# Kernel tuning notes

Hardware: AMD Instinct MI355X
Metric: run time of the kernel (lower is better)

The kernel has to match this reference:

```python
import jax, jax.numpy as jnp
import numpy as np

LN_EPS = 1e-5

def _layernorm(x, g, b):
    mu = jnp.mean(x, axis=-1, keepdims=True)
    var = jnp.mean((x - mu) ** 2, axis=-1, keepdims=True)
    return (x - mu) * jax.lax.rsqrt(var + LN_EPS) * g + b

def _linear_init(k, fan_in, fan_out):
    s = 1.0 / np.sqrt(fan_in)
    kw, kb = jax.random.split(k)
    W = jax.random.uniform(kw, (fan_in, fan_out), jnp.float32, -s, s)
    b = jax.random.uniform(kb, (fan_out,), jnp.float32, -s, s)
    return W, b

def setup_inputs() -> dict:
    key = jax.random.key(0)
    ks = jax.random.split(key, 8)
    B, C, H, W = 4, 256, 64, 64
    Cout = 256
    N = H * W
    E = 16 * N
    x = jax.random.normal(ks[0], (B, C, H, W), jnp.float32)
    edge_index = jax.random.randint(ks[1], (2, E), 0, N)
    W1, b1 = _linear_init(ks[2], C, 1024)
    W2, b2 = _linear_init(ks[3], 1024, 512)
    W3, b3 = _linear_init(ks[4], 512, Cout)
    return {
        'x': x, 'edge_index': edge_index,
        'W1': W1, 'b1': b1, 'g1': jnp.ones(1024, jnp.float32), 'be1': jnp.zeros(1024, jnp.float32),
        'W2': W2, 'b2': b2, 'g2': jnp.ones(512, jnp.float32), 'be2': jnp.zeros(512, jnp.float32),
        'W3': W3, 'b3': b3, 'g_out': jnp.ones(Cout, jnp.float32), 'b_out': jnp.zeros(Cout, jnp.float32),
    }

def reference(x, edge_index, W1, b1, g1, be1, W2, b2, g2, be2, W3, b3, g_out, b_out):
    B, C, H, Wd = x.shape
    N = H * Wd
    # [B, N, C] node features (pixels as nodes)
    x_flat = x.reshape(B, C, N).transpose(0, 2, 1)
    # Dense adjacency from edge list (duplicates sum, same as sparse->to_dense).
    # Identical for every batch item, so build once and broadcast through einsum.
    A = jnp.zeros((N, N), x.dtype).at[edge_index[0], edge_index[1]].add(1.0)
    A = A + jnp.eye(N, dtype=x.dtype)  # self-loops
    deg = jnp.sum(A, axis=-1)
    d_inv_sqrt = jnp.where(deg > 0, jax.lax.rsqrt(deg), 0.0)
    A_norm = d_inv_sqrt[:, None] * A * d_inv_sqrt[None, :]
    # message passing: [N,N] @ [B,N,C] -> [B,N,C]
    h = jnp.einsum('mn,bnc->bmc', A_norm, x_flat)
    h = _layernorm(jax.nn.relu(h @ W1 + b1), g1, be1)
    h = _layernorm(jax.nn.relu(h @ W2 + b2), g2, be2)
    h = h @ W3 + b3
    h = _layernorm(h, g_out, b_out)
    return h.transpose(0, 2, 1).reshape(B, -1, H, Wd)
```

## Files before the change

kernel.cpp:

```cpp
#include <hip/hip_runtime.h>

typedef __attribute__((ext_vector_type(8))) short short8_t;
typedef __attribute__((ext_vector_type(4))) float f32x4;

#define AS1 __attribute__((address_space(1)))
#define AS3 __attribute__((address_space(3)))

static_assert(sizeof(short8_t) == 16, "short8_t must be 16B");

__device__ __forceinline__ short f2bf(float f) {
  union { float f; unsigned u; } v; v.f = f;
  unsigned r = (v.u + 0x7FFFu + ((v.u >> 16) & 1u)) >> 16;
  return (short)r;
}
__device__ __forceinline__ float bf2f(short s) {
  union { unsigned u; float f; } v; v.u = ((unsigned)(unsigned short)s) << 16;
  return v.f;
}

__global__ __launch_bounds__(256) void zero_ws(int4* __restrict__ p, int n4) {
  const int i = blockIdx.x * 256 + threadIdx.x;
  if (i < n4) p[i] = int4{0, 0, 0, 0};
}

__global__ __launch_bounds__(256) void count_deg(const int* __restrict__ ei,
                                                 int* __restrict__ deg, int E) {
  int e = blockIdx.x * 256 + threadIdx.x;
  if (e < E) atomicAdd(&deg[ei[e]], 1);
}

__global__ __launch_bounds__(1024) void scan_deg(const int* __restrict__ deg,
                                                 int* __restrict__ rp,
                                                 float* __restrict__ dis) {
  __shared__ int part[1024];
  const int t = threadIdx.x;
  int4 v = ((const int4*)deg)[t];
  const int s = v.x + v.y + v.z + v.w;
  part[t] = s;
  __syncthreads();
  for (int off = 1; off < 1024; off <<= 1) {
    int mine = part[t];
    int add = (t >= off) ? part[t - off] : 0;
    __syncthreads();
    part[t] = mine + add;
    __syncthreads();
  }
  const int excl = part[t] - s;
  const int b4 = t * 4;
  rp[b4 + 0] = excl;
  rp[b4 + 1] = excl + v.x;
  rp[b4 + 2] = excl + v.x + v.y;
  rp[b4 + 3] = excl + v.x + v.y + v.z;
  if (t == 1023) rp[4096] = part[1023];
  dis[b4 + 0] = rsqrtf((float)(v.x + 1));
  dis[b4 + 1] = rsqrtf((float)(v.y + 1));
  dis[b4 + 2] = rsqrtf((float)(v.z + 1));
  dis[b4 + 3] = rsqrtf((float)(v.w + 1));
}

__global__ __launch_bounds__(256) void prep(
    const int* __restrict__ ei, const int* __restrict__ rp, int* __restrict__ fil,
    int* __restrict__ cols, int E,
    const float* __restrict__ x, const float* __restrict__ dis, short* __restrict__ xs,
    const float* __restrict__ W1, const float* __restrict__ W2, const float* __restrict__ W3,
    const float* __restrict__ g1, const float* __restrict__ be1,
    const float* __restrict__ g2, const float* __restrict__ be2,
    short* __restrict__ w1t, short* __restrict__ w2t, short* __restrict__ w3t,
    float* __restrict__ cs2, float* __restrict__ ct2,
    float* __restrict__ cs3, float* __restrict__ ct3) {
  __shared__ float tile[32][33];
  const int tx = threadIdx.x, ty = threadIdx.y;
  const int bid = blockIdx.x;
  if (bid < 256) {
    const int e = bid * 256 + ty * 32 + tx;
    if (e < E) {
      const int r = ei[e], c = ei[E + e];
      const int p = atomicAdd(&fil[r], 1);
      cols[rp[r] + p] = c;
    }
    return;
  }
  if (bid < 256 + 4096) {
    const int id = bid - 256;
    const int b = id >> 10;
    const int n0 = ((id & 1023) >> 3) * 32;
    const int c0 = (id & 7) * 32;
    const float* xb = x + (long)b * (256 * 4096);
#pragma unroll
    for (int i = 0; i < 32; i += 8)
      tile[ty + i][tx] = xb[(long)(c0 + ty + i) * 4096 + n0 + tx];
    __syncthreads();
#pragma unroll
    for (int i = 0; i < 32; i += 8) {
      const int n = n0 + ty + i;
      xs[(long)n * 1024 + b * 256 + c0 + tx] = f2bf(tile[tx][ty + i] * dis[n]);
    }
    return;
  }
  int id = bid - 4352;
  const float *Wf, *g = nullptr, *be = nullptr;
  float *cs = nullptr, *ctp = nullptr;
  short* Wt;
  int K, N, k0, n0;
  if (id < 256)      { Wf = W1; Wt = w1t; K = 256;  N = 1024; k0 = (id & 7) * 32;  n0 = (id >> 3) * 32; }
  else if (id < 768) { id -= 256; Wf = W2; Wt = w2t; K = 1024; N = 512; k0 = (id & 31) * 32; n0 = (id >> 5) * 32;
                       g = g1; be = be1; cs = cs2; ctp = ct2; }
  else               { id -= 768; Wf = W3; Wt = w3t; K = 512;  N = 256; k0 = (id & 15) * 32; n0 = (id >> 4) * 32;
                       g = g2; be = be2; cs = cs3; ctp = ct3; }
  float csp = 0.f, ctv = 0.f;
#pragma unroll
  for (int i = 0; i < 32; i += 8) {
    const int k = k0 + ty + i;
    const float wv = Wf[(long)k * N + n0 + tx];
    const float gk = g ? g[k] : 1.0f;
    tile[ty + i][tx] = gk * wv;
    csp += gk * wv;
    if (be) ctv += be[k] * wv;
  }
  __syncthreads();
#pragma unroll
  for (int i = 0; i < 32; i += 8)
    Wt[(long)(n0 + ty + i) * K + k0 + tx] = f2bf(tile[tx][ty + i]);
  if (cs) {
    atomicAdd(&cs[n0 + tx], csp);
    atomicAdd(&ctp[n0 + tx], ctv);
  }
}

__global__ __launch_bounds__(256) void gather_mp(const short* __restrict__ xs,
                                                 const float* __restrict__ dis,
                                                 const int* __restrict__ rp,
                                                 const int* __restrict__ cols,
                                                 short* __restrict__ h0) {
  __shared__ int sc[256];
  const int m = blockIdx.x;
  const int t = threadIdx.x;
  short4 v0 = ((const short4*)(xs + (long)m * 1024))[t];
  float a0 = bf2f(v0.x), a1 = bf2f(v0.y), a2 = bf2f(v0.z), a3 = bf2f(v0.w);
  const int s = rp[m], e = rp[m + 1];
  for (int base = s; base < e; base += 256) {
    const int cnt = min(256, e - base);
    __syncthreads();
    if (t < cnt) sc[t] = cols[base + t];
    __syncthreads();
    int j = 0;
    for (; j + 4 <= cnt; j += 4) {
      const int n0 = sc[j], n1 = sc[j + 1], n2 = sc[j + 2], n3 = sc[j + 3];
      short4 w0 = ((const short4*)(xs + (long)n0 * 1024))[t];
      short4 w1 = ((const short4*)(xs + (long)n1 * 1024))[t];
      short4 w2 = ((const short4*)(xs + (long)n2 * 1024))[t];
      short4 w3 = ((const short4*)(xs + (long)n3 * 1024))[t];
      a0 += bf2f(w0.x) + bf2f(w1.x) + bf2f(w2.x) + bf2f(w3.x);
      a1 += bf2f(w0.y) + bf2f(w1.y) + bf2f(w2.y) + bf2f(w3.y);
      a2 += bf2f(w0.z) + bf2f(w1.z) + bf2f(w2.z) + bf2f(w3.z);
      a3 += bf2f(w0.w) + bf2f(w1.w) + bf2f(w2.w) + bf2f(w3.w);
    }
    for (; j < cnt; ++j) {
      const int n = sc[j];
      short4 v = ((const short4*)(xs + (long)n * 1024))[t];
      a0 += bf2f(v.x); a1 += bf2f(v.y); a2 += bf2f(v.z); a3 += bf2f(v.w);
    }
  }
  const float d = dis[m];
  short4 o;
  o.x = f2bf(a0 * d); o.y = f2bf(a1 * d); o.z = f2bf(a2 * d); o.w = f2bf(a3 * d);
  const int b = t >> 6, c4 = t & 63;
  ((short4*)(h0 + (((long)b << 12) + m) * 256))[c4] = o;
}

template <bool LNIN, bool RELU>
__global__ __launch_bounds__(256, 3) void gemm_ln(
    const short* __restrict__ A, const short* __restrict__ Bt,
    const float* __restrict__ bias, const float* __restrict__ cs,
    const float* __restrict__ ct, const float* __restrict__ statsIn,
    float* __restrict__ statsOut, short* __restrict__ out,
    int M, int N, int K) {
  __shared__ __align__(16) short As[2][128 * 32];
  __shared__ __align__(16) short Bs[2][128 * 32];
  const int tid = threadIdx.x;
  const int lane = tid & 63;
  const int wave = tid >> 6;
  const int wm = wave >> 1, wn = wave & 1;
  const int m0 = blockIdx.x * 128, n0 = blockIdx.y * 128;

  f32x4 acc[4][4] = {};

  const int srow = wave * 32 + (lane >> 2);
  const int scol = (lane & 3) * 8;
  const short* ag = A + (long)(m0 + srow) * K + scol;
  const short* bg = Bt + (long)(n0 + srow) * K + scol;
  const int ldst = (wave * 32) * 32;
  const int fr = lane & 15;
  const int kc = (lane >> 4) * 8;
  const int NT = K >> 5;

#define STAGE(T, BUF)                                                                        \
  do {                                                                                       \
    const short* a_ = ag + (T) * 32;                                                         \
    const short* b_ = bg + (T) * 32;                                                         \
    __builtin_amdgcn_global_load_lds((const AS1 void*)a_, (AS3 void*)(&As[BUF][ldst]), 16, 0, 0); \
    __builtin_amdgcn_global_load_lds((const AS1 void*)(a_ + 16 * K), (AS3 void*)(&As[BUF][ldst + 512]), 16, 0, 0); \
    __builtin_amdgcn_global_load_lds((const AS1 void*)b_, (AS3 void*)(&Bs[BUF][ldst]), 16, 0, 0); \
    __builtin_amdgcn_global_load_lds((const AS1 void*)(b_ + 16 * K), (AS3 void*)(&Bs[BUF][ldst + 512]), 16, 0, 0); \
  } while (0)

  STAGE(0, 0);
  __syncthreads();
  int cur = 0;
  for (int t = 0; t < NT; ++t) {
    if (t + 1 < NT) STAGE(t + 1, cur ^ 1);
    short8_t af[4], bf[4];
#pragma unroll
    for (int i = 0; i < 4; ++i)
      af[i] = *(const short8_t*)&As[cur][(wm * 64 + i * 16 + fr) * 32 + kc];
#pragma unroll
    for (int i = 0; i < 4; ++i)
      bf[i] = *(const short8_t*)&Bs[cur][(wn * 64 + i * 16 + fr) * 32 + kc];
#pragma unroll
    for (int mi = 0; mi < 4; ++mi)
#pragma unroll
      for (int ni = 0; ni < 4; ++ni)
        acc[mi][ni] = __builtin_amdgcn_mfma_f32_16x16x32_bf16(af[mi], bf[ni],
                                                              acc[mi][ni], 0, 0, 0);
    __syncthreads();
    cur ^= 1;
  }
#undef STAGE

  const int rq = (lane >> 4) * 4;
  const float invK = 1.0f / (float)K;
  float bv[4], csv[4], ctv[4];
#pragma unroll
  for (int ni = 0; ni < 4; ++ni) {
    const int col = n0 + wn * 64 + ni * 16 + fr;
    bv[ni] = bias[col];
    if (LNIN) { csv[ni] = cs[col]; ctv[ni] = ct[col]; }
  }
#pragma unroll
  for (int mi = 0; mi < 4; ++mi) {
    float r1[4], rmu[4];
    if (LNIN) {
#pragma unroll
      for (int r = 0; r < 4; ++r) {
        const int row = m0 + wm * 64 + mi * 16 + rq + r;
        const float s = statsIn[row * 2];
        const float q = statsIn[row * 2 + 1];
        const float mu = s * invK;
        const float var = fmaxf(q * invK - mu * mu, 0.0f);
        const float rr = rsqrtf(var + 1e-5f);
        r1[r] = rr; rmu[r] = rr * mu;
      }
    }
    float sv[4] = {0, 0, 0, 0}, qv[4] = {0, 0, 0, 0};
#pragma unroll
    for (int ni = 0; ni < 4; ++ni) {
      const int col = n0 + wn * 64 + ni * 16 + fr;
#pragma unroll
      for (int r = 0; r < 4; ++r) {
        const int row = m0 + wm * 64 + mi * 16 + rq + r;
        float v = acc[mi][ni][r];
        if (LNIN) v = r1[r] * v - rmu[r] * csv[ni] + ctv[ni] + bv[ni];
        else      v = v + bv[ni];
        if (RELU) v = fmaxf(v, 0.0f);
        out[(long)row * N + col] = f2bf(v);
        sv[r] += v; qv[r] += v * v;
      }
    }
#pragma unroll
    for (int r = 0; r < 4; ++r) {
      float s = sv[r], q = qv[r];
#pragma unroll
      for (int off = 1; off < 16; off <<= 1) {
        s += __shfl_xor(s, off);
        q += __shfl_xor(q, off);
      }
      if (fr == 0) {
        const int row = m0 + wm * 64 + mi * 16 + rq + r;
        atomicAdd(&statsOut[row * 2], s);
        atomicAdd(&statsOut[row * 2 + 1], q);
      }
    }
  }
}

__global__ __launch_bounds__(256) void ln_tr_out(const short* __restrict__ t3,
                                                 const float* __restrict__ stats,
                                                 const float* __restrict__ g,
                                                 const float* __restrict__ be,
                                                 float* __restrict__ out) {
  __shared__ short tile[64][66];
  const int tx = threadIdx.x;
  const int ty = threadIdx.y;
  const int n0 = blockIdx.x * 64;
  const int c0 = blockIdx.y * 64;
  const int b = blockIdx.z;
  const long rbase = ((long)b << 12) + n0;
#pragma unroll
  for (int i = ty; i < 64; i += 4)
    tile[i][tx] = t3[(rbase + i) * 256 + c0 + tx];
  const float s = stats[(rbase + tx) * 2];
  const float q = stats[(rbase + tx) * 2 + 1];
  const float mu = s * (1.0f / 256.0f);
  const float var = fmaxf(q * (1.0f / 256.0f) - mu * mu, 0.0f);
  const float inv = rsqrtf(var + 1e-5f);
  __syncthreads();
  float* ob = out + ((long)b << 20) + n0 + tx;
#pragma unroll
  for (int i = ty; i < 64; i += 4) {
    const int c = c0 + i;
    ob[(long)c * 4096] = (bf2f(tile[tx][i]) - mu) * inv * g[c] + be[c];
  }
}

extern "C" void kernel_launch(void* const* d_in, const int* in_sizes, int n_in,
                              void* d_out, int out_size, void* d_ws, size_t ws_size,
                              hipStream_t stream) {
  (void)n_in; (void)out_size; (void)ws_size;
  const float* x   = (const float*)d_in[0];
  const int*   ei  = (const int*)d_in[1];
  const float* W1  = (const float*)d_in[2];
  const float* b1  = (const float*)d_in[3];
  const float* g1  = (const float*)d_in[4];
  const float* be1 = (const float*)d_in[5];
  const float* W2  = (const float*)d_in[6];
  const float* b2  = (const float*)d_in[7];
  const float* g2  = (const float*)d_in[8];
  const float* be2 = (const float*)d_in[9];
  const float* W3  = (const float*)d_in[10];
  const float* b3  = (const float*)d_in[11];
  const float* go  = (const float*)d_in[12];
  const float* bo  = (const float*)d_in[13];
  float* out = (float*)d_out;
  const int E = in_sizes[1] / 2;

  char* w = (char*)d_ws;
  int*   deg    = (int*)(w + 0);
  int*   fil    = (int*)(w + (16 << 10));
  float* stats1 = (float*)(w + (32 << 10));
  float* stats2 = (float*)(w + (160 << 10));
  float* stats3 = (float*)(w + (288 << 10));
  float* cs2    = (float*)(w + (416 << 10));
  float* ct2    = (float*)(w + (418 << 10));
  float* cs3    = (float*)(w + (420 << 10));
  float* ct3    = (float*)(w + (421 << 10));
  int*   rp   = (int*)(w + (424 << 10));
  float* dis  = (float*)(w + (444 << 10));
  int*   cols = (int*)(w + (460 << 10));
  short* w1t  = (short*)(w + (720 << 10));
  short* w2t  = (short*)(w + (1240 << 10));
  short* w3t  = (short*)(w + (2264 << 10));
  short* xs   = (short*)(w + (3ull << 20));
  short* h0   = (short*)(w + (11ull << 20));
  short* t1   = (short*)(w + (19ull << 20));
  short* t2   = (short*)(w + (51ull << 20));
  short* t3   = (short*)(w + (67ull << 20));

  const int n4 = (422 << 10) / 16;
  zero_ws<<<(n4 + 255) / 256, 256, 0, stream>>>((int4*)d_ws, n4);
  count_deg<<<256, 256, 0, stream>>>(ei, deg, E);
  scan_deg<<<1, 1024, 0, stream>>>(deg, rp, dis);
  prep<<<5248, dim3(32, 8), 0, stream>>>(ei, rp, fil, cols, E, x, dis, xs,
                                         W1, W2, W3, g1, be1, g2, be2,
                                         w1t, w2t, w3t, cs2, ct2, cs3, ct3);
  gather_mp<<<4096, 256, 0, stream>>>(xs, dis, rp, cols, h0);
  gemm_ln<false, true><<<dim3(128, 8), 256, 0, stream>>>(
      h0, w1t, b1, nullptr, nullptr, nullptr, stats1, t1, 16384, 1024, 256);
  gemm_ln<true, true><<<dim3(128, 4), 256, 0, stream>>>(
      t1, w2t, b2, cs2, ct2, stats1, stats2, t2, 16384, 512, 1024);
  gemm_ln<true, false><<<dim3(128, 2), 256, 0, stream>>>(
      t2, w3t, b3, cs3, ct3, stats2, stats3, t3, 16384, 256, 512);
  ln_tr_out<<<dim3(64, 4, 4), dim3(64, 4), 0, stream>>>(t3, stats3, go, bo, out);
}
```

Before: 147.5 us.

## Fuse final GEMM with output LayerNorm and transpose; enlarge GEMM1 M tile

The third GEMM becomes a dedicated kernel where each block owns 64 full rows of all 256 output columns. This lets the output LayerNorm statistics be reduced in registers, and normalized results are written directly in transposed NCHW layout. That removes the t3 intermediate round trip, the stats3 atomics and a separate kernel launch. The first GEMM also gets a 256x128 tile variant to improve reuse of the weight tile, at the cost of higher register pressure. The fused kernel launches only 256 blocks, which may leave compute units underused.

```diff
diff --git a/kernel.cpp b/kernel.cpp
--- a/kernel.cpp
+++ b/kernel.cpp
@@ -168,6 +168,102 @@
   ((short4*)(h0 + (((long)b << 12) + m) * 256))[c4] = o;
 }
 
+__global__ __launch_bounds__(256, 2) void gemm1_256(
+    const short* __restrict__ A, const short* __restrict__ Bt,
+    const float* __restrict__ bias, float* __restrict__ statsOut,
+    short* __restrict__ out, int M, int N, int K) {
+  __shared__ __align__(16) short As[2][256 * 32];
+  __shared__ __align__(16) short Bs[2][128 * 32];
+  const int tid = threadIdx.x;
+  const int lane = tid & 63;
+  const int wave = tid >> 6;
+  const int wm = wave >> 1, wn = wave & 1;
+  const int m0 = blockIdx.x * 256, n0 = blockIdx.y * 128;
+
+  f32x4 acc[8][4] = {};
+
+  const int srowA = wave * 64 + (lane >> 2);
+  const int srowB = wave * 32 + (lane >> 2);
+  const int scol = (lane & 3) * 8;
+  const short* ag = A + (long)(m0 + srowA) * K + scol;
+  const short* bg = Bt + (long)(n0 + srowB) * K + scol;
+  const int aslo = (wave * 64) * 32;
+  const int bslo = (wave * 32) * 32;
+  const int fr = lane & 15;
+  const int kc = (lane >> 4) * 8;
+  const int NT = K >> 5;
+
+#define STAGE(T, BUF)                                                                        \
+  do {                                                                                       \
+    const short* a_ = ag + (T) * 32;                                                         \
+    const short* b_ = bg + (T) * 32;                                                         \
+    _Pragma("unroll")                                                                        \
+    for (int i = 0; i < 4; ++i)                                                              \
+      __builtin_amdgcn_global_load_lds((const AS1 void*)(a_ + i * 16 * K),                   \
+                                       (AS3 void*)(&As[BUF][aslo + i * 512]), 16, 0, 0);     \
+    _Pragma("unroll")                                                                        \
+    for (int i = 0; i < 2; ++i)                                                              \
+      __builtin_amdgcn_global_load_lds((const AS1 void*)(b_ + i * 16 * K),                   \
+                                       (AS3 void*)(&Bs[BUF][bslo + i * 512]), 16, 0, 0);     \
+  } while (0)
+
+  STAGE(0, 0);
+  __syncthreads();
+  int cur = 0;
+  for (int t = 0; t < NT; ++t) {
+    if (t + 1 < NT) STAGE(t + 1, cur ^ 1);
+    short8_t bf[4];
+#pragma unroll
+    for (int i = 0; i < 4; ++i)
+      bf[i] = *(const short8_t*)&Bs[cur][(wn * 64 + i * 16 + fr) * 32 + kc];
+#pragma unroll
+    for (int mi = 0; mi < 8; ++mi) {
+      short8_t af = *(const short8_t*)&As[cur][(wm * 128 + mi * 16 + fr) * 32 + kc];
+#pragma unroll
+      for (int ni = 0; ni < 4; ++ni)
+        acc[mi][ni] = __builtin_amdgcn_mfma_f32_16x16x32_bf16(af, bf[ni],
+                                                              acc[mi][ni], 0, 0, 0);
+    }
+    __syncthreads();
+    cur ^= 1;
+  }
+#undef STAGE
+
+  const int rq = (lane >> 4) * 4;
+  float bv[4];
+#pragma unroll
+  for (int ni = 0; ni < 4; ++ni) bv[ni] = bias[n0 + wn * 64 + ni * 16 + fr];
+#pragma unroll
+  for (int mi = 0; mi < 8; ++mi) {
+    float sv[4] = {0, 0, 0, 0}, qv[4] = {0, 0, 0, 0};
+#pragma unroll
+    for (int ni = 0; ni < 4; ++ni) {
+      const int col = n0 + wn * 64 + ni * 16 + fr;
+#pragma unroll
+      for (int r = 0; r < 4; ++r) {
+        const int row = m0 + wm * 128 + mi * 16 + rq + r;
+        float v = fmaxf(acc[mi][ni][r] + bv[ni], 0.0f);
+        out[(long)row * N + col] = f2bf(v);
+        sv[r] += v; qv[r] += v * v;
+      }
+    }
+#pragma unroll
+    for (int r = 0; r < 4; ++r) {
+      float s = sv[r], q = qv[r];
+#pragma unroll
+      for (int off = 1; off < 16; off <<= 1) {
+        s += __shfl_xor(s, off);
+        q += __shfl_xor(q, off);
+      }
+      if (fr == 0) {
+        const int row = m0 + wm * 128 + mi * 16 + rq + r;
+        atomicAdd(&statsOut[row * 2], s);
+        atomicAdd(&statsOut[row * 2 + 1], q);
+      }
+    }
+  }
+}
+
 template <bool LNIN, bool RELU>
 __global__ __launch_bounds__(256, 3) void gemm_ln(
     const short* __restrict__ A, const short* __restrict__ Bt,
@@ -283,32 +379,111 @@
   }
 }
 
-__global__ __launch_bounds__(256) void ln_tr_out(const short* __restrict__ t3,
-                                                 const float* __restrict__ stats,
-                                                 const float* __restrict__ g,
-                                                 const float* __restrict__ be,
-                                                 float* __restrict__ out) {
-  __shared__ short tile[64][66];
-  const int tx = threadIdx.x;
-  const int ty = threadIdx.y;
-  const int n0 = blockIdx.x * 64;
-  const int c0 = blockIdx.y * 64;
-  const int b = blockIdx.z;
-  const long rbase = ((long)b << 12) + n0;
-#pragma unroll
-  for (int i = ty; i < 64; i += 4)
-    tile[i][tx] = t3[(rbase + i) * 256 + c0 + tx];
-  const float s = stats[(rbase + tx) * 2];
-  const float q = stats[(rbase + tx) * 2 + 1];
-  const float mu = s * (1.0f / 256.0f);
-  const float var = fmaxf(q * (1.0f / 256.0f) - mu * mu, 0.0f);
-  const float inv = rsqrtf(var + 1e-5f);
+__global__ __launch_bounds__(256, 2) void gemm3_ln_out(
+    const short* __restrict__ A, const short* __restrict__ Bt,
+    const float* __restrict__ bias, const float* __restrict__ cs,
+    const float* __restrict__ ct, const float* __restrict__ statsIn,
+    const float* __restrict__ go, const float* __restrict__ bo,
+    float* __restrict__ out) {
+  constexpr int K = 512, N = 256;
+  __shared__ __align__(16) short As[2][64 * 32];
+  __shared__ __align__(16) short Bs[2][256 * 32];
+  const int tid = threadIdx.x;
+  const int lane = tid & 63;
+  const int wave = tid >> 6;
+  const int m0 = blockIdx.x * 64;
+
+  f32x4 acc[16] = {};
+
+  const int srowA = wave * 16 + (lane >> 2);
+  const int srowB = wave * 64 + (lane >> 2);
+  const int scol = (lane & 3) * 8;
+  const short* ag = A + (long)(m0 + srowA) * K + scol;
+  const short* bg = Bt + (long)srowB * K + scol;
+  const int aslo = (wave * 16) * 32;
+  const int bslo = (wave * 64) * 32;
+  const int fr = lane & 15;
+  const int kc = (lane >> 4) * 8;
+  const int NT = K >> 5;
+
+#define STAGE(T, BUF)                                                                        \
+  do {                                                                                       \
+    const short* a_ = ag + (T) * 32;                                                         \
+    const short* b_ = bg + (T) * 32;                                                         \
+    __builtin_amdgcn_global_load_lds((const AS1 void*)a_, (AS3 void*)(&As[BUF][aslo]), 16, 0, 0); \
+    _Pragma("unroll")                                                                        \
+    for (int i = 0; i < 4; ++i)                                                              \
+      __builtin_amdgcn_global_load_lds((const AS1 void*)(b_ + i * 16 * K),                   \
+                                       (AS3 void*)(&Bs[BUF][bslo + i * 512]), 16, 0, 0);     \
+  } while (0)
+
+  STAGE(0, 0);
   __syncthreads();
-  float* ob = out + ((long)b << 20) + n0 + tx;
-#pragma unroll
-  for (int i = ty; i < 64; i += 4) {
-    const int c = c0 + i;
-    ob[(long)c * 4096] = (bf2f(tile[tx][i]) - mu) * inv * g[c] + be[c];
+  int cur = 0;
+  for (int t = 0; t < NT; ++t) {
+    if (t + 1 < NT) STAGE(t + 1, cur ^ 1);
+    short8_t af = *(const short8_t*)&As[cur][(wave * 16 + fr) * 32 + kc];
+#pragma unroll
+    for (int ni = 0; ni < 16; ++ni) {
+      short8_t bf = *(const short8_t*)&Bs[cur][(ni * 16 + fr) * 32 + kc];
+      acc[ni] = __builtin_amdgcn_mfma_f32_16x16x32_bf16(af, bf, acc[ni], 0, 0, 0);
+    }
+    __syncthreads();
+    cur ^= 1;
+  }
+#undef STAGE
+
+  const int rq = (lane >> 4) * 4;
+  float r1[4], rmu[4];
+#pragma unroll
+  for (int r = 0; r < 4; ++r) {
+    const int row = m0 + wave * 16 + rq + r;
+    const float s = statsIn[row * 2];
+    const float q = statsIn[row * 2 + 1];
+    const float mu = s * (1.0f / 512.0f);
+    const float var = fmaxf(q * (1.0f / 512.0f) - mu * mu, 0.0f);
+    const float rr = rsqrtf(var + 1e-5f);
+    r1[r] = rr; rmu[r] = rr * mu;
+  }
+  float sv[4] = {0, 0, 0, 0}, qv[4] = {0, 0, 0, 0};
+#pragma unroll
+  for (int ni = 0; ni < 16; ++ni) {
+    const int col = ni * 16 + fr;
+    const float bv = bias[col], csv = cs[col], ctv = ct[col];
+#pragma unroll
+    for (int r = 0; r < 4; ++r) {
+      const float v = r1[r] * acc[ni][r] - rmu[r] * csv + ctv + bv;
+      acc[ni][r] = v;
+      sv[r] += v; qv[r] += v * v;
+    }
+  }
+#pragma unroll
+  for (int off = 1; off < 16; off <<= 1) {
+#pragma unroll
+    for (int r = 0; r < 4; ++r) {
+      sv[r] += __shfl_xor(sv[r], off);
+      qv[r] += __shfl_xor(qv[r], off);
+    }
+  }
+  float mu[4], inv[4];
+#pragma unroll
+  for (int r = 0; r < 4; ++r) {
+    mu[r] = sv[r] * (1.0f / 256.0f);
+    const float var = fmaxf(qv[r] * (1.0f / 256.0f) - mu[r] * mu[r], 0.0f);
+    inv[r] = rsqrtf(var + 1e-5f);
+  }
+  const int b = m0 >> 12;
+  const int nbase = (m0 & 4095) + wave * 16 + rq;
+  float* ob = out + ((long)b << 20) + nbase;
+#pragma unroll
+  for (int ni = 0; ni < 16; ++ni) {
+    const int c = ni * 16 + fr;
+    const float gv = go[c], bv2 = bo[c];
+    f32x4 o;
+#pragma unroll
+    for (int r = 0; r < 4; ++r)
+      o[r] = (acc[ni][r] - mu[r]) * inv[r] * gv + bv2;
+    *(f32x4*)(ob + (long)c * 4096) = o;
   }
 }
 
@@ -338,7 +513,6 @@
   int*   fil    = (int*)(w + (16 << 10));
   float* stats1 = (float*)(w + (32 << 10));
   float* stats2 = (float*)(w + (160 << 10));
-  float* stats3 = (float*)(w + (288 << 10));
   float* cs2    = (float*)(w + (416 << 10));
   float* ct2    = (float*)(w + (418 << 10));
   float* cs3    = (float*)(w + (420 << 10));
@@ -353,7 +527,6 @@
   short* h0   = (short*)(w + (11ull << 20));
   short* t1   = (short*)(w + (19ull << 20));
   short* t2   = (short*)(w + (51ull << 20));
-  short* t3   = (short*)(w + (67ull << 20));
 
   const int n4 = (422 << 10) / 16;
   zero_ws<<<(n4 + 255) / 256, 256, 0, stream>>>((int4*)d_ws, n4);
@@ -363,11 +536,10 @@
                                          W1, W2, W3, g1, be1, g2, be2,
                                          w1t, w2t, w3t, cs2, ct2, cs3, ct3);
   gather_mp<<<4096, 256, 0, stream>>>(xs, dis, rp, cols, h0);
-  gemm_ln<false, true><<<dim3(128, 8), 256, 0, stream>>>(
-      h0, w1t, b1, nullptr, nullptr, nullptr, stats1, t1, 16384, 1024, 256);
+  gemm1_256<<<dim3(64, 8), 256, 0, stream>>>(h0, w1t, b1, stats1, t1,
+                                             16384, 1024, 256);
   gemm_ln<true, true><<<dim3(128, 4), 256, 0, stream>>>(
       t1, w2t, b2, cs2, ct2, stats1, stats2, t2, 16384, 512, 1024);
-  gemm_ln<true, false><<<dim3(128, 2), 256, 0, stream>>>(
-      t2, w3t, b3, cs3, ct3, stats2, stats3, t3, 16384, 256, 512);
-  ln_tr_out<<<dim3(64, 4, 4), dim3(64, 4), 0, stream>>>(t3, stats3, go, bo, out);
-}
+  gemm3_ln_out<<<256, 256, 0, stream>>>(t2, w3t, b3, cs3, ct3, stats2,
+                                        go, bo, out);
+}
```

Result: no change. 147.6 us (+0.0%).
